# Kernel optimization log

Hardware: AMD Instinct MI355X
Metric: run time of the kernel (lower is better)

Reference implementation:

```python
import jax, jax.numpy as jnp
import numpy as np

K = 64      # neighbor_num (subgraph size)
TOPK = 10   # topk for sparse adjacency scatter
DN = 10     # density_neighbor


def _build_graphs(indexes, features):
    # compute_knn: inner-product top-K neighbor table over all N samples
    N, D = features.shape
    sim = features @ features.T                      # [N, N]
    _, ori0 = jax.lax.top_k(sim, K)                  # [N, K] neighbor indices
    # density: all_sim[n] = sum_{i<DN} <f_n, f_{ori0[n,i]}> / (4*DN)
    g = features[ori0[:, :DN]]                       # [N, DN, D]
    all_sim = jnp.einsum('nd,nkd->n', features, g) / (4.0 * DN)
    exp_sim = jnp.exp(all_sim)                       # [N]

    rows = jnp.arange(K)[:, None]                    # [K,1]

    def build_one(idx):
        nbr = ori0[idx]                              # [K] neighbors of query idx
        feat = features[nbr]                         # [K, D]
        neigh = ori0[nbr][:, :TOPK]                  # [K, TOPK]
        A = (feat @ features.T) * exp_sim[None, :]   # [K, N] density-reweighted sims
        # scatter only the topk entries of each row into sparse tmp
        tmp = jnp.zeros((K, N), features.dtype).at[rows, neigh].set(A[rows, neigh])
        adj = tmp @ (tmp.T > 0).astype(features.dtype)   # [K, K]
        adj = jax.nn.softmax(adj, axis=1)
        x = feat - feat[0]                           # center on query node
        return x, adj

    return jax.vmap(build_one)(indexes)              # [B,K,D], [B,K,K]


def _gconv(x, adj, W, b):
    # GraphConv with MeanAggregator: out = relu(concat([x, adj@x]) @ W + b)
    agg = jnp.einsum('bij,bjd->bid', adj, x)
    cat = jnp.concatenate([x, agg], axis=-1)
    return jax.nn.relu(jnp.einsum('bkd,df->bkf', cat, W) + b)


def setup_inputs() -> dict:
    key = jax.random.key(0)
    ks = jax.random.split(key, 16)
    N, D, NHID = 8192, 2048, 1024
    feats = jax.random.normal(ks[0], (N, D), dtype=jnp.float32)
    feats = feats / jnp.linalg.norm(feats, axis=1, keepdims=True)  # L2-normalized embeddings
    p = lambda k, shape: jax.random.normal(k, shape, dtype=jnp.float32) * 0.02
    return {
        'indexes': jax.random.randint(ks[1], (64,), 0, N, dtype=jnp.int64) if jax.config.jax_enable_x64 else jax.random.randint(ks[1], (64,), 0, N, dtype=jnp.int32),
        'features': feats,
        'labels': jax.random.randint(ks[2], (N,), 0, 1000, dtype=jnp.int32),
        'domain': 1,
        'W1': p(ks[3], (2 * D, NHID)), 'b1': jnp.zeros((NHID,), jnp.float32),
        'W2': p(ks[4], (2 * NHID, 512)), 'b2': jnp.zeros((512,), jnp.float32),
        'W3': p(ks[5], (2 * 512, 256)), 'b3': jnp.zeros((256,), jnp.float32),
        'W4': p(ks[6], (2 * 256, 256)), 'b4': jnp.zeros((256,), jnp.float32),
        'Wc1': p(ks[7], (256, 256)), 'bc1': jnp.zeros((256,), jnp.float32),
        'prelu_a': jnp.full((256,), 0.25, jnp.float32),
        'Wc2': p(ks[8], (256, 2)), 'bc2': jnp.zeros((2,), jnp.float32),
    }


def reference(indexes, features, labels, domain, W1, b1, W2, b2, W3, b3, W4, b4,
              Wc1, bc1, prelu_a, Wc2, bc2):
    # labels only used for the (optional) loss branch; domain=1 path implemented.
    xs, adjs = _build_graphs(indexes, features)      # built under no_grad in torch
    h = _gconv(xs, adjs, W1, b1)
    h = _gconv(h, adjs, W2, b2)
    h = _gconv(h, adjs, W3, b3)
    h = _gconv(h, adjs, W4, b4)
    h = h @ Wc1 + bc1
    h = jnp.where(h > 0, h, prelu_a * h)             # PReLU(256)
    pred = h @ Wc2 + bc2                             # [B, K, 2]
    return pred
```

## Files before the change

### kernel.cpp

```cpp
#include <hip/hip_runtime.h>
#include <hip/hip_bf16.h>
#include <math.h>

#define NROWS 8192
#define DFEAT 2048
#define KSEL  64
#define CHK   2048

typedef unsigned long long u64;
typedef __attribute__((ext_vector_type(8))) short bf16x8;
typedef __attribute__((ext_vector_type(4))) float f32x4;

__device__ __forceinline__ u64 umax64(u64 a, u64 b) { return a > b ? a : b; }

__device__ __forceinline__ void split2(float v, ushort& h, ushort& l) {
  __hip_bfloat16 bh = __float2bfloat16(v);
  float r = v - __bfloat162float(bh);
  __hip_bfloat16 bl = __float2bfloat16(r);
  h = *(ushort*)&bh; l = *(ushort*)&bl;
}

__device__ __forceinline__ u64 mkkey_vi(float v, int i) {
  unsigned u = __float_as_uint(v);
  u = ((int)u < 0) ? ~u : (u | 0x80000000u);
  return ((u64)u << 32) | (u64)(0xFFFFFFFFu - (unsigned)i);
}

__global__ __launch_bounds__(256) void k_split(const float* __restrict__ F, ushort* __restrict__ H,
                                               ushort* __restrict__ M, ushort* __restrict__ L) {
  const size_t i0 = ((size_t)blockIdx.x * 256 + threadIdx.x) * 4;
  float4 x = *(const float4*)(F + i0);
  float xs[4] = {x.x, x.y, x.z, x.w};
  ushort h[4], m[4], l[4];
#pragma unroll
  for (int c = 0; c < 4; ++c) {
    float v = xs[c];
    __hip_bfloat16 bh = __float2bfloat16(v);
    float r1 = v - __bfloat162float(bh);
    __hip_bfloat16 bm = __float2bfloat16(r1);
    float r2 = r1 - __bfloat162float(bm);
    __hip_bfloat16 bl = __float2bfloat16(r2);
    h[c] = *(ushort*)&bh; m[c] = *(ushort*)&bm; l[c] = *(ushort*)&bl;
  }
  ushort4 vh = {h[0], h[1], h[2], h[3]};
  ushort4 vm = {m[0], m[1], m[2], m[3]};
  ushort4 vl = {l[0], l[1], l[2], l[3]};
  *(ushort4*)(H + i0) = vh;
  *(ushort4*)(M + i0) = vm;
  *(ushort4*)(L + i0) = vl;
}

__global__ __launch_bounds__(256) void k_simgemm_pair(
    const ushort* __restrict__ FH, const ushort* __restrict__ FM, const ushort* __restrict__ FL,
    float* __restrict__ T0, float* __restrict__ T0T, int i0, int j0, int d0,
    float* __restrict__ T1, float* __restrict__ T1T, int i1, int j1, int d1) {
  __shared__ ushort lds[6 * 4096];
  const int z = blockIdx.z;
  float* TILE = z ? T1 : T0;
  float* TILT = z ? T1T : T0T;
  const int ci = z ? i1 : i0;
  const int cj = z ? j1 : j0;
  const int diag = z ? d1 : d0;
  const int bj = blockIdx.x;
  const int bm = blockIdx.y;
  if (diag && bm > bj) return;
  const int t = threadIdx.x;
  const int w = t >> 6, l = t & 63;
  const int arow0 = ci * CHK + bm * 128;
  const int brow0 = cj * CHK + bj * 128;
  const int segr = l >> 2;
  const int segq_s = (l & 3) ^ ((l >> 3) & 3);
  const int fl15 = l & 15, fq = l >> 4;
  const int kswz = (fq ^ ((fl15 >> 1) & 3)) * 8;
  const int wr = w >> 1, wc = w & 1;
  const int mb = wr * 64, nb = wc * 64;

  f32x4 acc[4][4];
#pragma unroll
  for (int i = 0; i < 4; ++i)
#pragma unroll
    for (int j = 0; j < 4; ++j) acc[i][j] = (f32x4){0.f, 0.f, 0.f, 0.f};

  for (int k0 = 0; k0 < DFEAT; k0 += 32) {
    __syncthreads();
#pragma unroll
    for (int c = 0; c < 12; ++c) {
      const int cc = w * 12 + c;
      const int tt = cc >> 3;
      const int p = cc & 7;
      const int rowbase = (tt < 3) ? arow0 : brow0;
      const int sp = (tt < 3) ? tt : (tt - 3);
      const ushort* sel = (sp == 0) ? FH : ((sp == 1) ? FM : FL);
      const ushort* g = sel + (size_t)(rowbase + p * 16 + segr) * DFEAT + (k0 + segq_s * 8);
      __builtin_amdgcn_global_load_lds((const __attribute__((address_space(1))) unsigned int*)g,
                                       (__attribute__((address_space(3))) unsigned int*)&lds[tt * 4096 + p * 512],
                                       16, 0, 0);
    }
    __syncthreads();

    bf16x8 af[3][4];
    bf16x8 bg[3][4];
#pragma unroll
    for (int i = 0; i < 3; ++i)
#pragma unroll
      for (int fm = 0; fm < 4; ++fm)
        af[i][fm] = *(const bf16x8*)&lds[i * 4096 + (mb + fm * 16 + fl15) * 32 + kswz];
#pragma unroll
    for (int j = 0; j < 3; ++j)
#pragma unroll
      for (int fn = 0; fn < 4; ++fn)
        bg[j][fn] = *(const bf16x8*)&lds[(3 + j) * 4096 + (nb + fn * 16 + fl15) * 32 + kswz];

#pragma unroll
    for (int fm = 0; fm < 4; ++fm)
#pragma unroll
      for (int fn = 0; fn < 4; ++fn) {
        f32x4 a = acc[fm][fn];
        a = __builtin_amdgcn_mfma_f32_16x16x32_bf16(af[0][fm], bg[0][fn], a, 0, 0, 0);
        a = __builtin_amdgcn_mfma_f32_16x16x32_bf16(af[1][fm], bg[0][fn], a, 0, 0, 0);
        a = __builtin_amdgcn_mfma_f32_16x16x32_bf16(af[0][fm], bg[1][fn], a, 0, 0, 0);
        a = __builtin_amdgcn_mfma_f32_16x16x32_bf16(af[2][fm], bg[0][fn], a, 0, 0, 0);
        a = __builtin_amdgcn_mfma_f32_16x16x32_bf16(af[0][fm], bg[2][fn], a, 0, 0, 0);
        a = __builtin_amdgcn_mfma_f32_16x16x32_bf16(af[1][fm], bg[1][fn], a, 0, 0, 0);
        acc[fm][fn] = a;
      }
  }

  const bool doT = (TILT != nullptr) && !(diag && bm == bj);
#pragma unroll
  for (int fm = 0; fm < 4; ++fm) {
    const int lm = bm * 128 + mb + fm * 16 + fq * 4;
#pragma unroll
    for (int fn = 0; fn < 4; ++fn) {
      const int col = bj * 128 + nb + fn * 16 + fl15;
#pragma unroll
      for (int r = 0; r < 4; ++r)
        TILE[(size_t)(lm + r) * CHK + col] = acc[fm][fn][r];
      if (doT) {
        float4 v = make_float4(acc[fm][fn][0], acc[fm][fn][1], acc[fm][fn][2], acc[fm][fn][3]);
        *(float4*)(TILT + (size_t)col * CHK + lm) = v;
      }
    }
  }
}

__global__ __launch_bounds__(256) void k_simgemm_mfma(
    const ushort* __restrict__ FH, const ushort* __restrict__ FM, const ushort* __restrict__ FL,
    float* __restrict__ C, int row0) {
  __shared__ ushort lds[6 * 4096];
  const int bj = blockIdx.x;
  const int bm = blockIdx.y;
  const int t = threadIdx.x;
  const int w = t >> 6, l = t & 63;
  const int arow0 = row0 + bm * 128;
  const int brow0 = bj * 128;
  const int segr = l >> 2;
  const int segq = l & 3;
  const int fl15 = l & 15, fq = l >> 4;
  const int wr = w >> 1, wc = w & 1;
  const int mb = wr * 64, nb = wc * 64;

  f32x4 acc[4][4];
#pragma unroll
  for (int i = 0; i < 4; ++i)
#pragma unroll
    for (int j = 0; j < 4; ++j) acc[i][j] = (f32x4){0.f, 0.f, 0.f, 0.f};

  for (int k0 = 0; k0 < DFEAT; k0 += 32) {
    __syncthreads();
#pragma unroll
    for (int c = 0; c < 12; ++c) {
      const int cc = w * 12 + c;
      const int tt = cc >> 3;
      const int p = cc & 7;
      const int rowbase = (tt < 3) ? arow0 : brow0;
      const int sp = (tt < 3) ? tt : (tt - 3);
      const ushort* sel = (sp == 0) ? FH : ((sp == 1) ? FM : FL);
      const ushort* g = sel + (size_t)(rowbase + p * 16 + segr) * DFEAT + (k0 + segq * 8);
      __builtin_amdgcn_global_load_lds((const __attribute__((address_space(1))) unsigned int*)g,
                                       (__attribute__((address_space(3))) unsigned int*)&lds[tt * 4096 + p * 512],
                                       16, 0, 0);
    }
    __syncthreads();

    bf16x8 af[3][4];
    bf16x8 bg[3][4];
    const int kcol = fq * 8;
#pragma unroll
    for (int i = 0; i < 3; ++i)
#pragma unroll
      for (int fm = 0; fm < 4; ++fm)
        af[i][fm] = *(const bf16x8*)&lds[i * 4096 + (mb + fm * 16 + fl15) * 32 + kcol];
#pragma unroll
    for (int j = 0; j < 3; ++j)
#pragma unroll
      for (int fn = 0; fn < 4; ++fn)
        bg[j][fn] = *(const bf16x8*)&lds[(3 + j) * 4096 + (nb + fn * 16 + fl15) * 32 + kcol];

#pragma unroll
    for (int fm = 0; fm < 4; ++fm)
#pragma unroll
      for (int fn = 0; fn < 4; ++fn) {
        f32x4 a = acc[fm][fn];
        a = __builtin_amdgcn_mfma_f32_16x16x32_bf16(af[0][fm], bg[0][fn], a, 0, 0, 0);
        a = __builtin_amdgcn_mfma_f32_16x16x32_bf16(af[1][fm], bg[0][fn], a, 0, 0, 0);
        a = __builtin_amdgcn_mfma_f32_16x16x32_bf16(af[0][fm], bg[1][fn], a, 0, 0, 0);
        a = __builtin_amdgcn_mfma_f32_16x16x32_bf16(af[2][fm], bg[0][fn], a, 0, 0, 0);
        a = __builtin_amdgcn_mfma_f32_16x16x32_bf16(af[0][fm], bg[2][fn], a, 0, 0, 0);
        a = __builtin_amdgcn_mfma_f32_16x16x32_bf16(af[1][fm], bg[1][fn], a, 0, 0, 0);
        acc[fm][fn] = a;
      }
  }

#pragma unroll
  for (int fm = 0; fm < 4; ++fm) {
    const int lm = bm * 128 + mb + fm * 16 + fq * 4;
#pragma unroll
    for (int fn = 0; fn < 4; ++fn) {
      const int col = bj * 128 + nb + fn * 16 + fl15;
#pragma unroll
      for (int r = 0; r < 4; ++r)
        C[(size_t)(lm + r) * NROWS + col] = acc[fm][fn][r];
    }
  }
}

__global__ __launch_bounds__(256) void k_gemm3(const ushort* __restrict__ AH, const ushort* __restrict__ AL,
                                               const ushort* __restrict__ BH, const ushort* __restrict__ BL,
                                               float* __restrict__ C, int K, int N) {
  __shared__ ushort lds[4 * 4096];
  const int bj = blockIdx.x, bm = blockIdx.y;
  const int t = threadIdx.x;
  const int w = t >> 6, l = t & 63;
  const int segr = l >> 2;
  const int segq_s = (l & 3) ^ ((l >> 3) & 3);
  const int fl15 = l & 15, fq = l >> 4;
  const int kswz = (fq ^ ((fl15 >> 1) & 3)) * 8;
  const int wr = w >> 1, wc = w & 1;
  const int mb = wr * 64, nb = wc * 64;

  f32x4 acc[4][4];
#pragma unroll
  for (int i = 0; i < 4; ++i)
#pragma unroll
    for (int j = 0; j < 4; ++j) acc[i][j] = (f32x4){0.f, 0.f, 0.f, 0.f};

  for (int k0 = 0; k0 < K; k0 += 32) {
    __syncthreads();
#pragma unroll
    for (int c = 0; c < 8; ++c) {
      const int s = w * 8 + c;
      const int tt = s >> 3;
      const int p = s & 7;
      const int rowbase = (tt < 2) ? (bm * 128) : (bj * 128);
      const ushort* sel = (tt == 0) ? AH : ((tt == 1) ? AL : ((tt == 2) ? BH : BL));
      const ushort* g = sel + (size_t)(rowbase + p * 16 + segr) * K + (k0 + segq_s * 8);
      __builtin_amdgcn_global_load_lds((const __attribute__((address_space(1))) unsigned int*)g,
                                       (__attribute__((address_space(3))) unsigned int*)&lds[s * 512],
                                       16, 0, 0);
    }
    __syncthreads();

    bf16x8 af[2][4];
    bf16x8 bg[2][4];
#pragma unroll
    for (int i = 0; i < 2; ++i)
#pragma unroll
      for (int fm = 0; fm < 4; ++fm)
        af[i][fm] = *(const bf16x8*)&lds[i * 4096 + (mb + fm * 16 + fl15) * 32 + kswz];
#pragma unroll
    for (int j = 0; j < 2; ++j)
#pragma unroll
      for (int fn = 0; fn < 4; ++fn)
        bg[j][fn] = *(const bf16x8*)&lds[(2 + j) * 4096 + (nb + fn * 16 + fl15) * 32 + kswz];

#pragma unroll
    for (int fm = 0; fm < 4; ++fm)
#pragma unroll
      for (int fn = 0; fn < 4; ++fn) {
        f32x4 a = acc[fm][fn];
        a = __builtin_amdgcn_mfma_f32_16x16x32_bf16(af[0][fm], bg[0][fn], a, 0, 0, 0);
        a = __builtin_amdgcn_mfma_f32_16x16x32_bf16(af[0][fm], bg[1][fn], a, 0, 0, 0);
        a = __builtin_amdgcn_mfma_f32_16x16x32_bf16(af[1][fm], bg[0][fn], a, 0, 0, 0);
        acc[fm][fn] = a;
      }
  }

#pragma unroll
  for (int fm = 0; fm < 4; ++fm) {
    const int row = bm * 128 + mb + fm * 16 + fq * 4;
#pragma unroll
    for (int fn = 0; fn < 4; ++fn) {
      const int col = bj * 128 + nb + fn * 16 + fl15;
#pragma unroll
      for (int r = 0; r < 4; ++r)
        C[(size_t)(row + r) * N + col] = acc[fm][fn][r];
    }
  }
}

__global__ __launch_bounds__(256) void k_init_topk(float* __restrict__ topv, int* __restrict__ topi) {
  const int i = blockIdx.x * 256 + threadIdx.x;
  topv[i] = -INFINITY;
  topi[i] = 0;
}

__global__ __launch_bounds__(256) void k_topk_update(const float* __restrict__ T, int rowbase, int colbase,
                                                     float* __restrict__ topv, int* __restrict__ topi) {
  __shared__ unsigned cnt[64];
  __shared__ unsigned nsel;
  __shared__ u64 selbuf[64];
  const int t = threadIdx.x;
  const int row = rowbase + blockIdx.x;
  const float* src = T + (size_t)blockIdx.x * CHK;

  if (t < 64) cnt[t] = 0;
  if (t == 0) nsel = 0;

  u64 k[9];
  int nk = 8;
#pragma unroll
  for (int q = 0; q < 8; ++q) {
    float v = src[t + 256 * q];
    k[q] = mkkey_vi(v, colbase + t + 256 * q);
  }
  k[8] = 0;
  if (t < 64) {
    k[8] = mkkey_vi(topv[(size_t)row * KSEL + t], topi[(size_t)row * KSEL + t]);
    nk = 9;
  }
  __syncthreads();

  u64 T64 = 0;
  for (int bit = 63; bit >= 0; --bit) {
    const u64 cand = T64 | (1ull << bit);
    unsigned c = 0;
#pragma unroll
    for (int q = 0; q < 9; ++q) c += (q < nk && k[q] >= cand) ? 1u : 0u;
#pragma unroll
    for (int s = 32; s > 0; s >>= 1) c += __shfl_down(c, s);
    if ((t & 63) == 0) atomicAdd(&cnt[bit], c);
    __syncthreads();
    const unsigned cb = cnt[bit];
    if (cb >= 64) T64 = cand;
    if (cb == 64) break;
  }

#pragma unroll
  for (int q = 0; q < 9; ++q) {
    if (q < nk && k[q] >= T64) {
      unsigned p = atomicAdd(&nsel, 1u);
      if (p < 64) selbuf[p] = k[q];
    }
  }
  __syncthreads();

  if (t < 64) {
    u64 key = selbuf[t];
#pragma unroll
    for (int kk = 2; kk <= 64; kk <<= 1) {
#pragma unroll
      for (int j = kk >> 1; j > 0; j >>= 1) {
        u64 other = __shfl_xor(key, j);
        const bool dirDesc = ((t & kk) == 0);
        const bool upper = ((t & j) != 0);
        u64 mx = umax64(key, other);
        u64 mn = (key < other) ? key : other;
        key = (dirDesc ^ upper) ? mx : mn;
      }
    }
    const unsigned ui = (unsigned)(key >> 32);
    const float v = __uint_as_float((ui & 0x80000000u) ? (ui ^ 0x80000000u) : ~ui);
    const int idx = (int)(0xFFFFFFFFu - (unsigned)(key & 0xFFFFFFFFull));
    topv[(size_t)row * KSEL + t] = v;
    topi[(size_t)row * KSEL + t] = idx;
  }
}

__global__ __launch_bounds__(256) void k_exps(const float* __restrict__ topv, float* __restrict__ exps) {
  const int r = blockIdx.x * 256 + threadIdx.x;
  float s = 0.f;
#pragma unroll
  for (int q = 0; q < 10; ++q) s += topv[(size_t)r * KSEL + q];
  exps[r] = expf(s / 40.0f);
}

__global__ __launch_bounds__(256) void k_topk(const float* __restrict__ simc,
                                              float* __restrict__ topv, int* __restrict__ topi,
                                              float* __restrict__ exps, int row0) {
  __shared__ float vals[NROWS];
  __shared__ u64 wmax[4];
  __shared__ float outv[KSEL];
  __shared__ int outi[KSEL];
  const int row = row0 + blockIdx.x;
  const int t = threadIdx.x;
  const float* src = simc + (size_t)blockIdx.x * NROWS;
  for (int i = t; i < NROWS; i += 256) vals[i] = src[i];
  __syncthreads();

  u64 lk = 0;
#pragma unroll
  for (int m = 0; m < 32; ++m) {
    int i = t + 256 * m;
    lk = umax64(lk, mkkey_vi(vals[i], i));
  }

  const int lane = t & 63, wv = t >> 6;
  for (int it = 0; it < KSEL; ++it) {
    u64 wk = lk;
#pragma unroll
    for (int s = 32; s > 0; s >>= 1) {
      u64 o = __shfl_xor(wk, s);
      wk = umax64(wk, o);
    }
    if (lane == 0) wmax[wv] = wk;
    __syncthreads();
    u64 g = umax64(umax64(wmax[0], wmax[1]), umax64(wmax[2], wmax[3]));
    const unsigned ui = (unsigned)(g >> 32);
    const float v = __uint_as_float((ui & 0x80000000u) ? (ui ^ 0x80000000u) : ~ui);
    const int idx = (int)(0xFFFFFFFFu - (unsigned)(g & 0xFFFFFFFFull));
    if (t == 0) { outv[it] = v; outi[it] = idx; }
    if (t == (idx & 255)) {
      vals[idx] = -INFINITY;
      u64 nl = 0;
#pragma unroll
      for (int m = 0; m < 32; ++m) {
        int i = t + 256 * m;
        nl = umax64(nl, mkkey_vi(vals[i], i));
      }
      lk = nl;
    }
    __syncthreads();
  }
  if (t < KSEL) {
    topv[(size_t)row * KSEL + t] = outv[t];
    topi[(size_t)row * KSEL + t] = outi[t];
  }
  if (t == 0) {
    float s = 0.f;
#pragma unroll
    for (int q = 0; q < 10; ++q) s += outv[q];
    exps[row] = expf(s / 40.0f);
  }
}

__global__ __launch_bounds__(256) void k_adj(const int* __restrict__ indexes,
                                             const float* __restrict__ topv, const int* __restrict__ topi,
                                             const float* __restrict__ exps, float* __restrict__ adj) {
  __shared__ int nbr[64];
  __shared__ int neigh[64][10];
  __shared__ float tv[64][10];
  __shared__ float adjL[64][64];
  const int b = blockIdx.x;
  const int t = threadIdx.x;
  const int idx = indexes[b];
  if (t < 64) nbr[t] = topi[(size_t)idx * KSEL + t];
  __syncthreads();
  for (int p = t; p < 640; p += 256) {
    const int r = p / 10, q = p - r * 10;
    const int m = nbr[r];
    const int c = topi[(size_t)m * KSEL + q];
    neigh[r][q] = c;
    tv[r][q] = topv[(size_t)m * KSEL + q] * exps[c];
  }
  __syncthreads();
  for (int p = t; p < 4096; p += 256) {
    const int i = p >> 6, j = p & 63;
    float s = 0.f;
#pragma unroll
    for (int q = 0; q < 10; ++q) {
      const int c = neigh[i][q];
      float add = 0.f;
      for (int s2 = 0; s2 < 10; ++s2) {
        if (neigh[j][s2] == c) { add = (tv[j][s2] > 0.f) ? tv[i][q] : 0.f; break; }
      }
      s += add;
    }
    adjL[i][j] = s;
  }
  __syncthreads();
  const int wv = t >> 6, lane = t & 63;
  for (int i = wv * 16; i < wv * 16 + 16; ++i) {
    float v = adjL[i][lane];
    float mx = v;
#pragma unroll
    for (int s = 32; s > 0; s >>= 1) mx = fmaxf(mx, __shfl_xor(mx, s));
    float e = expf(v - mx);
    float sum = e;
#pragma unroll
    for (int s = 32; s > 0; s >>= 1) sum += __shfl_xor(sum, s);
    adj[((size_t)b * 64 + i) * 64 + lane] = e / sum;
  }
}

__global__ __launch_bounds__(256) void k_xs_split(const int* __restrict__ indexes, const int* __restrict__ topi,
                                                  const float* __restrict__ F,
                                                  ushort* __restrict__ XH, ushort* __restrict__ XL) {
  const int b = blockIdx.y, r = blockIdx.x;
  const int t = threadIdx.x;
  const int idx = indexes[b];
  const int m  = topi[(size_t)idx * KSEL + r];
  const int m0 = topi[(size_t)idx * KSEL + 0];
  const float4* pa = (const float4*)(F + (size_t)m * DFEAT);
  const float4* pb = (const float4*)(F + (size_t)m0 * DFEAT);
  const size_t rowoff = ((size_t)b * 64 + r) * DFEAT;
#pragma unroll
  for (int it = 0; it < 2; ++it) {
    const int i = t + it * 256;
    float4 a = pa[i], c = pb[i];
    float d[4] = {a.x - c.x, a.y - c.y, a.z - c.z, a.w - c.w};
    ushort h[4], l[4];
#pragma unroll
    for (int q = 0; q < 4; ++q) split2(d[q], h[q], l[q]);
    ushort4 vh = {h[0], h[1], h[2], h[3]};
    ushort4 vl = {l[0], l[1], l[2], l[3]};
    *(ushort4*)(XH + rowoff + i * 4) = vh;
    *(ushort4*)(XL + rowoff + i * 4) = vl;
  }
}

__global__ __launch_bounds__(256) void k_wsplitT(const float* __restrict__ W,
                                                 ushort* __restrict__ WTH, ushort* __restrict__ WTL,
                                                 int K, int F) {
  __shared__ float tile[32][33];
  const int k0 = blockIdx.x * 32;
  const int n0 = blockIdx.y * 32;
  const int t = threadIdx.x;
  {
    const int r = t >> 3, cq = t & 7;
    const int srcRow = (n0 < F) ? (k0 + r) : (K + k0 + r);
    const int srcCol = (n0 < F) ? n0 : (n0 - F);
    float4 v = *(const float4*)(W + (size_t)srcRow * F + srcCol + cq * 4);
    tile[r][cq * 4 + 0] = v.x; tile[r][cq * 4 + 1] = v.y;
    tile[r][cq * 4 + 2] = v.z; tile[r][cq * 4 + 3] = v.w;
  }
  __syncthreads();
  {
    const int nl = t >> 3, kq = t & 7;
    ushort h[4], l[4];
#pragma unroll
    for (int i = 0; i < 4; ++i) split2(tile[kq * 4 + i][nl], h[i], l[i]);
    ushort4 vh = {h[0], h[1], h[2], h[3]};
    ushort4 vl = {l[0], l[1], l[2], l[3]};
    *(ushort4*)(WTH + (size_t)(n0 + nl) * K + k0 + kq * 4) = vh;
    *(ushort4*)(WTL + (size_t)(n0 + nl) * K + k0 + kq * 4) = vl;
  }
}

__global__ __launch_bounds__(256) void k_postlayer(const float* __restrict__ C, const float* __restrict__ adj,
                                                   const float* __restrict__ bias,
                                                   ushort* __restrict__ HH, ushort* __restrict__ HL, int F) {
  __shared__ float adjL[64 * 65];
  __shared__ float QL[64 * 66];
  const int f0 = blockIdx.x * 64;
  const int b = blockIdx.y;
  const int t = threadIdx.x;
  const int fc = t & 63, rg = t >> 6;
  const int twoF = 2 * F;
  for (int i = t; i < 4096; i += 256) {
    const int r = i >> 6, j = i & 63;
    adjL[r * 65 + j] = adj[(size_t)b * 4096 + i];
    QL[r * 66 + j] = C[(size_t)(b * 64 + r) * twoF + F + f0 + j];
  }
  __syncthreads();
  const float bv = bias[f0 + fc];
  for (int rr = 0; rr < 16; ++rr) {
    const int r = rg * 16 + rr;
    float s = 0.f;
#pragma unroll 8
    for (int j0 = 0; j0 < 64; ++j0) {
      const int j = (j0 + fc) & 63;
      s += adjL[r * 65 + j] * QL[j * 66 + fc];
    }
    const int row = b * 64 + r;
    float h = C[(size_t)row * twoF + f0 + fc] + s + bv;
    h = fmaxf(h, 0.f);
    ushort hh, hl;
    split2(h, hh, hl);
    HH[(size_t)row * F + f0 + fc] = hh;
    HL[(size_t)row * F + f0 + fc] = hl;
  }
}

__global__ __launch_bounds__(256) void k_postcls(const float* __restrict__ C, const float* __restrict__ bias,
                                                 const float* __restrict__ pre, float* __restrict__ HC) {
  const size_t i0 = ((size_t)blockIdx.x * 256 + threadIdx.x) * 4;
  const int col = (int)(i0 & 255);
  float4 c = *(const float4*)(C + i0);
  float o[4] = {c.x, c.y, c.z, c.w};
#pragma unroll
  for (int i = 0; i < 4; ++i) {
    float h = o[i] + bias[col + i];
    o[i] = (h > 0.f) ? h : pre[col + i] * h;
  }
  *(float4*)(HC + i0) = make_float4(o[0], o[1], o[2], o[3]);
}

__global__ __launch_bounds__(256) void k_final(const float* __restrict__ Hc, const float* __restrict__ Wc2,
                                               const float* __restrict__ bc2, float* __restrict__ outp) {
  __shared__ float w[512];
  __shared__ float red[512];
  const int t = threadIdx.x;
  for (int i = t; i < 512; i += 256) w[i] = Wc2[i];
  __syncthreads();
  const int m = blockIdx.x * 64 + (t >> 2);
  const int p = t & 3;
  const float* h = Hc + (size_t)m * 256;
  float s0 = 0.f, s1 = 0.f;
  for (int k = p * 64; k < p * 64 + 64; ++k) {
    float hv = h[k];
    s0 += hv * w[k * 2];
    s1 += hv * w[k * 2 + 1];
  }
  red[t * 2] = s0; red[t * 2 + 1] = s1;
  __syncthreads();
  if (p == 0) {
    for (int q = 1; q < 4; ++q) { s0 += red[(t + q) * 2]; s1 += red[(t + q) * 2 + 1]; }
    outp[m * 2 + 0] = s0 + bc2[0];
    outp[m * 2 + 1] = s1 + bc2[1];
  }
}

extern "C" void kernel_launch(void* const* d_in, const int* in_sizes, int n_in,
                              void* d_out, int out_size, void* d_ws, size_t ws_size,
                              hipStream_t stream) {
  const int*   indexes = (const int*)d_in[0];
  const float* F   = (const float*)d_in[1];
  const float* W1  = (const float*)d_in[4];
  const float* b1  = (const float*)d_in[5];
  const float* W2  = (const float*)d_in[6];
  const float* b2  = (const float*)d_in[7];
  const float* W3  = (const float*)d_in[8];
  const float* b3  = (const float*)d_in[9];
  const float* W4  = (const float*)d_in[10];
  const float* b4  = (const float*)d_in[11];
  const float* Wc1 = (const float*)d_in[12];
  const float* bc1 = (const float*)d_in[13];
  const float* pre = (const float*)d_in[14];
  const float* Wc2 = (const float*)d_in[15];
  const float* bc2 = (const float*)d_in[16];
  float* out = (float*)d_out;

  size_t off = 0;
  auto take = [&](size_t bytes) -> char* {
    char* q = (char*)d_ws + off;
    off += (bytes + 255) & ~(size_t)255;
    return q;
  };
  float* TOPV = (float*)take((size_t)NROWS * KSEL * 4);
  int*   TOPI = (int*)  take((size_t)NROWS * KSEL * 4);
  float* EXPS = (float*)take((size_t)NROWS * 4);
  float* ADJ  = (float*)take((size_t)64 * 64 * 64 * 4);
  char*  big  = (char*)d_ws + off;
  const size_t big_bytes = (ws_size > off) ? (ws_size - off) : 0;

  const size_t Mi = 1024 * 1024;
  const size_t Ki = 1024;
  const size_t splitBytes = (size_t)NROWS * DFEAT * 2;

  if (big_bytes >= 160 * Mi) {
    ushort* FH = (ushort*)big;
    ushort* FM = (ushort*)(big + splitBytes);
    ushort* FL = (ushort*)(big + 2 * splitBytes);
    float* TILE0  = (float*)(big + 96 * Mi);
    float* TILE0T = (float*)(big + 112 * Mi);
    float* TILE1  = (float*)(big + 128 * Mi);
    float* TILE1T = (float*)(big + 144 * Mi);
    k_split<<<NROWS * DFEAT / 1024, 256, 0, stream>>>(F, FH, FM, FL);
    k_init_topk<<<NROWS * KSEL / 256, 256, 0, stream>>>(TOPV, TOPI);
    const int pairs[10][2] = {{0,0},{0,1},{0,2},{0,3},{1,1},{1,2},{1,3},{2,2},{2,3},{3,3}};
    for (int b = 0; b < 5; ++b) {
      const int ia = pairs[2*b][0],   ja = pairs[2*b][1];
      const int ib = pairs[2*b+1][0], jb = pairs[2*b+1][1];
      const int da = (ia == ja), db = (ib == jb);
      k_simgemm_pair<<<dim3(16, 16, 2), 256, 0, stream>>>(
          FH, FM, FL,
          TILE0, da ? TILE0 : TILE0T, ia, ja, da,
          TILE1, db ? TILE1 : TILE1T, ib, jb, db);
      k_topk_update<<<CHK, 256, 0, stream>>>(TILE0, ia * CHK, ja * CHK, TOPV, TOPI);
      if (!da) k_topk_update<<<CHK, 256, 0, stream>>>(TILE0T, ja * CHK, ia * CHK, TOPV, TOPI);
      k_topk_update<<<CHK, 256, 0, stream>>>(TILE1, ib * CHK, jb * CHK, TOPV, TOPI);
      if (!db) k_topk_update<<<CHK, 256, 0, stream>>>(TILE1T, jb * CHK, ib * CHK, TOPV, TOPI);
    }
    k_exps<<<NROWS / 256, 256, 0, stream>>>(TOPV, EXPS);
  } else {
    int fchunk = 0;
    for (int c = 2048; c >= 512; c >>= 1) {
      if (3 * splitBytes + (size_t)c * NROWS * 4 <= big_bytes) { fchunk = c; break; }
    }
    if (fchunk == 0) {
      hipMemsetAsync(d_out, 0, (size_t)out_size * 4, stream);
      return;
    }
    ushort* FH = (ushort*)big;
    ushort* FM = (ushort*)(big + splitBytes);
    ushort* FL = (ushort*)(big + 2 * splitBytes);
    float* SIMC = (float*)(big + 3 * splitBytes);
    k_split<<<NROWS * DFEAT / 1024, 256, 0, stream>>>(F, FH, FM, FL);
    for (int r0 = 0; r0 < NROWS; r0 += fchunk) {
      k_simgemm_mfma<<<dim3(64, fchunk / 128), 256, 0, stream>>>(FH, FM, FL, SIMC, r0);
      k_topk<<<fchunk, 256, 0, stream>>>(SIMC, TOPV, TOPI, EXPS, r0);
    }
  }
  k_adj<<<64, 256, 0, stream>>>(indexes, TOPV, TOPI, EXPS, ADJ);

  ushort* XH   = (ushort*)(big);
  ushort* XL   = (ushort*)(big + 16 * Mi);
  ushort* WT1H = (ushort*)(big + 32 * Mi);
  ushort* WT1L = (ushort*)(big + 40 * Mi);
  ushort* WT2H = (ushort*)(big + 48 * Mi);
  ushort* WT2L = (ushort*)(big + 50 * Mi);
  ushort* WT3H = (ushort*)(big + 52 * Mi);
  ushort* WT3L = (ushort*)(big + 52 * Mi + 512 * Ki);
  ushort* WT4H = (ushort*)(big + 53 * Mi);
  ushort* WT4L = (ushort*)(big + 53 * Mi + 256 * Ki);
  ushort* WTcH = (ushort*)(big + 53 * Mi + 512 * Ki);
  ushort* WTcL = (ushort*)(big + 53 * Mi + 640 * Ki);
  float*  CBUF = (float*)(big + 54 * Mi);
  float*  HC   = (float*)(big + 86 * Mi);
  ushort* H1H  = (ushort*)(big + 32 * Mi);
  ushort* H1L  = (ushort*)(big + 40 * Mi);
  ushort* H2H  = (ushort*)(big);
  ushort* H2L  = (ushort*)(big + 4 * Mi);
  ushort* H3H  = (ushort*)(big + 8 * Mi);
  ushort* H3L  = (ushort*)(big + 10 * Mi);
  ushort* H4H  = (ushort*)(big + 12 * Mi);
  ushort* H4L  = (ushort*)(big + 14 * Mi);

  k_wsplitT<<<dim3(2048 / 32, 2048 / 32), 256, 0, stream>>>(W1, WT1H, WT1L, 2048, 1024);
  k_wsplitT<<<dim3(1024 / 32, 1024 / 32), 256, 0, stream>>>(W2, WT2H, WT2L, 1024, 512);
  k_wsplitT<<<dim3(512 / 32, 512 / 32), 256, 0, stream>>>(W3, WT3H, WT3L, 512, 256);
  k_wsplitT<<<dim3(256 / 32, 512 / 32), 256, 0, stream>>>(W4, WT4H, WT4L, 256, 256);
  k_wsplitT<<<dim3(256 / 32, 256 / 32), 256, 0, stream>>>(Wc1, WTcH, WTcL, 256, 256);

  k_xs_split<<<dim3(64, 64), 256, 0, stream>>>(indexes, TOPI, F, XH, XL);

  k_gemm3<<<dim3(16, 32), 256, 0, stream>>>(XH, XL, WT1H, WT1L, CBUF, 2048, 2048);
  k_postlayer<<<dim3(16, 64), 256, 0, stream>>>(CBUF, ADJ, b1, H1H, H1L, 1024);
  k_gemm3<<<dim3(8, 32), 256, 0, stream>>>(H1H, H1L, WT2H, WT2L, CBUF, 1024, 1024);
  k_postlayer<<<dim3(8, 64), 256, 0, stream>>>(CBUF, ADJ, b2, H2H, H2L, 512);
  k_gemm3<<<dim3(4, 32), 256, 0, stream>>>(H2H, H2L, WT3H, WT3L, CBUF, 512, 512);
  k_postlayer<<<dim3(4, 64), 256, 0, stream>>>(CBUF, ADJ, b3, H3H, H3L, 256);
  k_gemm3<<<dim3(4, 32), 256, 0, stream>>>(H3H, H3L, WT4H, WT4L, CBUF, 256, 512);
  k_postlayer<<<dim3(4, 64), 256, 0, stream>>>(CBUF, ADJ, b4, H4H, H4L, 256);
  k_gemm3<<<dim3(2, 32), 256, 0, stream>>>(H4H, H4L, WTcH, WTcL, CBUF, 256, 256);
  k_postcls<<<4096 * 256 / 1024, 256, 0, stream>>>(CBUF, bc1, pre, HC);

  k_final<<<64, 256, 0, stream>>>(HC, Wc2, bc2, out);
}
```

Baseline: 1.650 ms.

## Compute all similarity tiles in one launch and batch top-k merges; fuse classifier epilogue

When the workspace is large enough, a single launch now computes all ten upper-triangular 2048x2048 similarity tiles, writing each tile and its transpose into a full 16-tile buffer. Top-k merges then run in four launches, each covering one tile per row-chunk. This replaces five paired GEMM launches plus many small per-tile top-k launches, giving more parallelism per launch and fewer launch gaps, at the cost of about 256MB of extra workspace. Separately, the bias+PReLU pass is folded into the final classifier kernel, removing one launch and an intermediate buffer.

```diff
diff --git a/kernel.cpp b/kernel.cpp
--- a/kernel.cpp
+++ b/kernel.cpp
@@ -48,6 +48,101 @@
   *(ushort4*)(H + i0) = vh;
   *(ushort4*)(M + i0) = vm;
   *(ushort4*)(L + i0) = vl;
+}
+
+__global__ __launch_bounds__(256) void k_simgemm_all(
+    const ushort* __restrict__ FH, const ushort* __restrict__ FM, const ushort* __restrict__ FL,
+    float* __restrict__ bufbase) {
+  __shared__ ushort lds[6 * 4096];
+  const int z = blockIdx.z;
+  int ci = 0, rem = z;
+  while (rem >= 4 - ci) { rem -= 4 - ci; ++ci; }
+  const int cj = ci + rem;
+  const int diag = (ci == cj);
+  const int bj = blockIdx.x;
+  const int bm = blockIdx.y;
+  if (diag && bm > bj) return;
+  const size_t TSZ = (size_t)CHK * CHK;
+  float* TILE = bufbase + (size_t)(ci * 4 + cj) * TSZ;
+  float* TILT = bufbase + (size_t)(cj * 4 + ci) * TSZ;
+  const int t = threadIdx.x;
+  const int w = t >> 6, l = t & 63;
+  const int arow0 = ci * CHK + bm * 128;
+  const int brow0 = cj * CHK + bj * 128;
+  const int segr = l >> 2;
+  const int segq_s = (l & 3) ^ ((l >> 3) & 3);
+  const int fl15 = l & 15, fq = l >> 4;
+  const int kswz = (fq ^ ((fl15 >> 1) & 3)) * 8;
+  const int wr = w >> 1, wc = w & 1;
+  const int mb = wr * 64, nb = wc * 64;
+
+  f32x4 acc[4][4];
+#pragma unroll
+  for (int i = 0; i < 4; ++i)
+#pragma unroll
+    for (int j = 0; j < 4; ++j) acc[i][j] = (f32x4){0.f, 0.f, 0.f, 0.f};
+
+  for (int k0 = 0; k0 < DFEAT; k0 += 32) {
+    __syncthreads();
+#pragma unroll
+    for (int c = 0; c < 12; ++c) {
+      const int cc = w * 12 + c;
+      const int tt = cc >> 3;
+      const int p = cc & 7;
+      const int rowbase = (tt < 3) ? arow0 : brow0;
+      const int sp = (tt < 3) ? tt : (tt - 3);
+      const ushort* sel = (sp == 0) ? FH : ((sp == 1) ? FM : FL);
+      const ushort* g = sel + (size_t)(rowbase + p * 16 + segr) * DFEAT + (k0 + segq_s * 8);
+      __builtin_amdgcn_global_load_lds((const __attribute__((address_space(1))) unsigned int*)g,
+                                       (__attribute__((address_space(3))) unsigned int*)&lds[tt * 4096 + p * 512],
+                                       16, 0, 0);
+    }
+    __syncthreads();
+
+    bf16x8 af[3][4];
+    bf16x8 bg[3][4];
+#pragma unroll
+    for (int i = 0; i < 3; ++i)
+#pragma unroll
+      for (int fm = 0; fm < 4; ++fm)
+        af[i][fm] = *(const bf16x8*)&lds[i * 4096 + (mb + fm * 16 + fl15) * 32 + kswz];
+#pragma unroll
+    for (int j = 0; j < 3; ++j)
+#pragma unroll
+      for (int fn = 0; fn < 4; ++fn)
+        bg[j][fn] = *(const bf16x8*)&lds[(3 + j) * 4096 + (nb + fn * 16 + fl15) * 32 + kswz];
+
+#pragma unroll
+    for (int fm = 0; fm < 4; ++fm)
+#pragma unroll
+      for (int fn = 0; fn < 4; ++fn) {
+        f32x4 a = acc[fm][fn];
+        a = __builtin_amdgcn_mfma_f32_16x16x32_bf16(af[0][fm], bg[0][fn], a, 0, 0, 0);
+        a = __builtin_amdgcn_mfma_f32_16x16x32_bf16(af[1][fm], bg[0][fn], a, 0, 0, 0);
+        a = __builtin_amdgcn_mfma_f32_16x16x32_bf16(af[0][fm], bg[1][fn], a, 0, 0, 0);
+        a = __builtin_amdgcn_mfma_f32_16x16x32_bf16(af[2][fm], bg[0][fn], a, 0, 0, 0);
+        a = __builtin_amdgcn_mfma_f32_16x16x32_bf16(af[0][fm], bg[2][fn], a, 0, 0, 0);
+        a = __builtin_amdgcn_mfma_f32_16x16x32_bf16(af[1][fm], bg[1][fn], a, 0, 0, 0);
+        acc[fm][fn] = a;
+      }
+  }
+
+  const bool doT = !(diag && bm == bj);
+#pragma unroll
+  for (int fm = 0; fm < 4; ++fm) {
+    const int lm = bm * 128 + mb + fm * 16 + fq * 4;
+#pragma unroll
+    for (int fn = 0; fn < 4; ++fn) {
+      const int col = bj * 128 + nb + fn * 16 + fl15;
+#pragma unroll
+      for (int r = 0; r < 4; ++r)
+        TILE[(size_t)(lm + r) * CHK + col] = acc[fm][fn][r];
+      if (doT) {
+        float4 v = make_float4(acc[fm][fn][0], acc[fm][fn][1], acc[fm][fn][2], acc[fm][fn][3]);
+        *(float4*)(TILT + (size_t)col * CHK + lm) = v;
+      }
+    }
+  }
 }
 
 __global__ __launch_bounds__(256) void k_simgemm_pair(
@@ -305,17 +400,12 @@
   topi[i] = 0;
 }
 
-__global__ __launch_bounds__(256) void k_topk_update(const float* __restrict__ T, int rowbase, int colbase,
-                                                     float* __restrict__ topv, int* __restrict__ topi) {
-  __shared__ unsigned cnt[64];
-  __shared__ unsigned nsel;
-  __shared__ u64 selbuf[64];
-  const int t = threadIdx.x;
-  const int row = rowbase + blockIdx.x;
-  const float* src = T + (size_t)blockIdx.x * CHK;
-
+__device__ __forceinline__ void topk_merge_body(const float* src, int row, int colbase,
+                                                float* topv, int* topi,
+                                                unsigned* cnt, unsigned* nselp, u64* selbuf) {
+  const int t = threadIdx.x;
   if (t < 64) cnt[t] = 0;
-  if (t == 0) nsel = 0;
+  if (t == 0) *nselp = 0;
 
   u64 k[9];
   int nk = 8;
@@ -349,7 +439,7 @@
 #pragma unroll
   for (int q = 0; q < 9; ++q) {
     if (q < nk && k[q] >= T64) {
-      unsigned p = atomicAdd(&nsel, 1u);
+      unsigned p = atomicAdd(nselp, 1u);
       if (p < 64) selbuf[p] = k[q];
     }
   }
@@ -377,6 +467,27 @@
   }
 }
 
+__global__ __launch_bounds__(256) void k_topk_update4(const float* __restrict__ bufbase, int g,
+                                                      float* __restrict__ topv, int* __restrict__ topi) {
+  __shared__ unsigned cnt[64];
+  __shared__ unsigned nsel;
+  __shared__ u64 selbuf[64];
+  const int r = blockIdx.y;
+  const int c = (r + g) & 3;
+  const size_t TSZ = (size_t)CHK * CHK;
+  const float* src = bufbase + (size_t)(r * 4 + c) * TSZ + (size_t)blockIdx.x * CHK;
+  topk_merge_body(src, r * CHK + blockIdx.x, c * CHK, topv, topi, cnt, &nsel, selbuf);
+}
+
+__global__ __launch_bounds__(256) void k_topk_update(const float* __restrict__ T, int rowbase, int colbase,
+                                                     float* __restrict__ topv, int* __restrict__ topi) {
+  __shared__ unsigned cnt[64];
+  __shared__ unsigned nsel;
+  __shared__ u64 selbuf[64];
+  const float* src = T + (size_t)blockIdx.x * CHK;
+  topk_merge_body(src, rowbase + blockIdx.x, colbase, topv, topi, cnt, &nsel, selbuf);
+}
+
 __global__ __launch_bounds__(256) void k_exps(const float* __restrict__ topv, float* __restrict__ exps) {
   const int r = blockIdx.x * 256 + threadIdx.x;
   float s = 0.f;
@@ -582,22 +693,9 @@
   }
 }
 
-__global__ __launch_bounds__(256) void k_postcls(const float* __restrict__ C, const float* __restrict__ bias,
-                                                 const float* __restrict__ pre, float* __restrict__ HC) {
-  const size_t i0 = ((size_t)blockIdx.x * 256 + threadIdx.x) * 4;
-  const int col = (int)(i0 & 255);
-  float4 c = *(const float4*)(C + i0);
-  float o[4] = {c.x, c.y, c.z, c.w};
-#pragma unroll
-  for (int i = 0; i < 4; ++i) {
-    float h = o[i] + bias[col + i];
-    o[i] = (h > 0.f) ? h : pre[col + i] * h;
-  }
-  *(float4*)(HC + i0) = make_float4(o[0], o[1], o[2], o[3]);
-}
-
-__global__ __launch_bounds__(256) void k_final(const float* __restrict__ Hc, const float* __restrict__ Wc2,
-                                               const float* __restrict__ bc2, float* __restrict__ outp) {
+__global__ __launch_bounds__(256) void k_final2(const float* __restrict__ C, const float* __restrict__ bc1,
+                                                const float* __restrict__ pre, const float* __restrict__ Wc2,
+                                                const float* __restrict__ bc2, float* __restrict__ outp) {
   __shared__ float w[512];
   __shared__ float red[512];
   const int t = threadIdx.x;
@@ -605,10 +703,11 @@
   __syncthreads();
   const int m = blockIdx.x * 64 + (t >> 2);
   const int p = t & 3;
-  const float* h = Hc + (size_t)m * 256;
+  const float* h = C + (size_t)m * 256;
   float s0 = 0.f, s1 = 0.f;
   for (int k = p * 64; k < p * 64 + 64; ++k) {
-    float hv = h[k];
+    float hv = h[k] + bc1[k];
+    hv = (hv > 0.f) ? hv : pre[k] * hv;
     s0 += hv * w[k * 2];
     s1 += hv * w[k * 2 + 1];
   }
@@ -658,7 +757,18 @@
   const size_t Ki = 1024;
   const size_t splitBytes = (size_t)NROWS * DFEAT * 2;
 
-  if (big_bytes >= 160 * Mi) {
+  if (big_bytes >= 352 * Mi) {
+    ushort* FH = (ushort*)big;
+    ushort* FM = (ushort*)(big + splitBytes);
+    ushort* FL = (ushort*)(big + 2 * splitBytes);
+    float* BUFS = (float*)(big + 96 * Mi);
+    k_split<<<NROWS * DFEAT / 1024, 256, 0, stream>>>(F, FH, FM, FL);
+    k_init_topk<<<NROWS * KSEL / 256, 256, 0, stream>>>(TOPV, TOPI);
+    k_simgemm_all<<<dim3(16, 16, 10), 256, 0, stream>>>(FH, FM, FL, BUFS);
+    for (int g = 0; g < 4; ++g)
+      k_topk_update4<<<dim3(CHK, 4), 256, 0, stream>>>(BUFS, g, TOPV, TOPI);
+    k_exps<<<NROWS / 256, 256, 0, stream>>>(TOPV, EXPS);
+  } else if (big_bytes >= 160 * Mi) {
     ushort* FH = (ushort*)big;
     ushort* FM = (ushort*)(big + splitBytes);
     ushort* FL = (ushort*)(big + 2 * splitBytes);
@@ -717,7 +827,6 @@
   ushort* WTcH = (ushort*)(big + 53 * Mi + 512 * Ki);
   ushort* WTcL = (ushort*)(big + 53 * Mi + 640 * Ki);
   float*  CBUF = (float*)(big + 54 * Mi);
-  float*  HC   = (float*)(big + 86 * Mi);
   ushort* H1H  = (ushort*)(big + 32 * Mi);
   ushort* H1L  = (ushort*)(big + 40 * Mi);
   ushort* H2H  = (ushort*)(big);
@@ -744,7 +853,5 @@
   k_gemm3<<<dim3(4, 32), 256, 0, stream>>>(H3H, H3L, WT4H, WT4L, CBUF, 256, 512);
   k_postlayer<<<dim3(4, 64), 256, 0, stream>>>(CBUF, ADJ, b4, H4H, H4L, 256);
   k_gemm3<<<dim3(2, 32), 256, 0, stream>>>(H4H, H4L, WTcH, WTcL, CBUF, 256, 256);
-  k_postcls<<<4096 * 256 / 1024, 256, 0, stream>>>(CBUF, bc1, pre, HC);
-
-  k_final<<<64, 256, 0, stream>>>(HC, Wc2, bc2, out);
-}
+  k_final2<<<64, 256, 0, stream>>>(CBUF, bc1, pre, Wc2, bc2, out);
+}
```

New measurement: 1.661 ms. Within noise of the previous version (+0.7%).

## Batch similarity tiles into fewer launches and fuse classifier epilogue

Applied to the files above, without the earlier changes.

Reworks the blocked similarity/top-k schedule so several 2048x2048 tile products run in one launch of up to six tiles, using a pool of tile buffers. The top-k merges are batched four chunks per launch, so the 8192 rows update in parallel instead of through many small launches. This needs a larger scratch buffer (224 MiB path) and keeps a fallback for 160 MiB. Separately, the bias+PReLU post-classifier kernel is folded into the final projection kernel, removing one pass over the 4096x256 buffer.

```diff
diff --git a/kernel.cpp b/kernel.cpp
--- a/kernel.cpp
+++ b/kernel.cpp
@@ -50,20 +50,21 @@
   *(ushort4*)(L + i0) = vl;
 }
 
-__global__ __launch_bounds__(256) void k_simgemm_pair(
+__global__ __launch_bounds__(256) void k_sim_batch(
     const ushort* __restrict__ FH, const ushort* __restrict__ FM, const ushort* __restrict__ FL,
-    float* __restrict__ T0, float* __restrict__ T0T, int i0, int j0, int d0,
-    float* __restrict__ T1, float* __restrict__ T1T, int i1, int j1, int d1) {
+    float* __restrict__ BUFS, int e0, int e1, int e2, int e3, int e4, int e5) {
   __shared__ ushort lds[6 * 4096];
   const int z = blockIdx.z;
-  float* TILE = z ? T1 : T0;
-  float* TILT = z ? T1T : T0T;
-  const int ci = z ? i1 : i0;
-  const int cj = z ? j1 : j0;
-  const int diag = z ? d1 : d0;
+  const int e = (z == 0) ? e0 : ((z == 1) ? e1 : ((z == 2) ? e2 : ((z == 3) ? e3 : ((z == 4) ? e4 : e5))));
+  const int ci = e & 15, cj = (e >> 4) & 15;
+  const int bA = (e >> 8) & 15, bB = (e >> 12) & 15;
+  const int diag = (e >> 16) & 1;
   const int bj = blockIdx.x;
   const int bm = blockIdx.y;
   if (diag && bm > bj) return;
+  const size_t TSZ = (size_t)CHK * CHK;
+  float* TILE = BUFS + (size_t)bA * TSZ;
+  float* TILT = BUFS + (size_t)bB * TSZ;
   const int t = threadIdx.x;
   const int w = t >> 6, l = t & 63;
   const int arow0 = ci * CHK + bm * 128;
@@ -85,9 +86,9 @@
     __syncthreads();
 #pragma unroll
     for (int c = 0; c < 12; ++c) {
-      const int cc = w * 12 + c;
-      const int tt = cc >> 3;
-      const int p = cc & 7;
+      const int cidx = w * 12 + c;
+      const int tt = cidx >> 3;
+      const int p = cidx & 7;
       const int rowbase = (tt < 3) ? arow0 : brow0;
       const int sp = (tt < 3) ? tt : (tt - 3);
       const ushort* sel = (sp == 0) ? FH : ((sp == 1) ? FM : FL);
@@ -126,7 +127,7 @@
       }
   }
 
-  const bool doT = (TILT != nullptr) && !(diag && bm == bj);
+  const bool doT = !(diag && bm == bj);
 #pragma unroll
   for (int fm = 0; fm < 4; ++fm) {
     const int lm = bm * 128 + mb + fm * 16 + fq * 4;
@@ -305,17 +306,12 @@
   topi[i] = 0;
 }
 
-__global__ __launch_bounds__(256) void k_topk_update(const float* __restrict__ T, int rowbase, int colbase,
-                                                     float* __restrict__ topv, int* __restrict__ topi) {
-  __shared__ unsigned cnt[64];
-  __shared__ unsigned nsel;
-  __shared__ u64 selbuf[64];
-  const int t = threadIdx.x;
-  const int row = rowbase + blockIdx.x;
-  const float* src = T + (size_t)blockIdx.x * CHK;
-
+__device__ __forceinline__ void topk_merge_body(const float* src, int row, int colbase,
+                                                float* topv, int* topi,
+                                                unsigned* cnt, unsigned* nselp, u64* selbuf) {
+  const int t = threadIdx.x;
   if (t < 64) cnt[t] = 0;
-  if (t == 0) nsel = 0;
+  if (t == 0) *nselp = 0;
 
   u64 k[9];
   int nk = 8;
@@ -349,7 +345,7 @@
 #pragma unroll
   for (int q = 0; q < 9; ++q) {
     if (q < nk && k[q] >= T64) {
-      unsigned p = atomicAdd(&nsel, 1u);
+      unsigned p = atomicAdd(nselp, 1u);
       if (p < 64) selbuf[p] = k[q];
     }
   }
@@ -377,6 +373,21 @@
   }
 }
 
+__global__ __launch_bounds__(256) void k_topk_upd4(const float* __restrict__ bufbase,
+                                                   int b0, int b1, int b2, int b3,
+                                                   int c0, int c1, int c2, int c3,
+                                                   float* __restrict__ topv, int* __restrict__ topi) {
+  __shared__ unsigned cnt[64];
+  __shared__ unsigned nsel;
+  __shared__ u64 selbuf[64];
+  const int y = blockIdx.y;
+  const int bi = (y == 0) ? b0 : ((y == 1) ? b1 : ((y == 2) ? b2 : b3));
+  const int cc = (y == 0) ? c0 : ((y == 1) ? c1 : ((y == 2) ? c2 : c3));
+  const size_t TSZ = (size_t)CHK * CHK;
+  const float* src = bufbase + (size_t)bi * TSZ + (size_t)blockIdx.x * CHK;
+  topk_merge_body(src, y * CHK + blockIdx.x, cc * CHK, topv, topi, cnt, &nsel, selbuf);
+}
+
 __global__ __launch_bounds__(256) void k_exps(const float* __restrict__ topv, float* __restrict__ exps) {
   const int r = blockIdx.x * 256 + threadIdx.x;
   float s = 0.f;
@@ -582,22 +593,9 @@
   }
 }
 
-__global__ __launch_bounds__(256) void k_postcls(const float* __restrict__ C, const float* __restrict__ bias,
-                                                 const float* __restrict__ pre, float* __restrict__ HC) {
-  const size_t i0 = ((size_t)blockIdx.x * 256 + threadIdx.x) * 4;
-  const int col = (int)(i0 & 255);
-  float4 c = *(const float4*)(C + i0);
-  float o[4] = {c.x, c.y, c.z, c.w};
-#pragma unroll
-  for (int i = 0; i < 4; ++i) {
-    float h = o[i] + bias[col + i];
-    o[i] = (h > 0.f) ? h : pre[col + i] * h;
-  }
-  *(float4*)(HC + i0) = make_float4(o[0], o[1], o[2], o[3]);
-}
-
-__global__ __launch_bounds__(256) void k_final(const float* __restrict__ Hc, const float* __restrict__ Wc2,
-                                               const float* __restrict__ bc2, float* __restrict__ outp) {
+__global__ __launch_bounds__(256) void k_final2(const float* __restrict__ C, const float* __restrict__ bc1,
+                                                const float* __restrict__ pre, const float* __restrict__ Wc2,
+                                                const float* __restrict__ bc2, float* __restrict__ outp) {
   __shared__ float w[512];
   __shared__ float red[512];
   const int t = threadIdx.x;
@@ -605,10 +603,11 @@
   __syncthreads();
   const int m = blockIdx.x * 64 + (t >> 2);
   const int p = t & 3;
-  const float* h = Hc + (size_t)m * 256;
+  const float* h = C + (size_t)m * 256;
   float s0 = 0.f, s1 = 0.f;
   for (int k = p * 64; k < p * 64 + 64; ++k) {
-    float hv = h[k];
+    float hv = h[k] + bc1[k];
+    hv = (hv > 0.f) ? hv : pre[k] * hv;
     s0 += hv * w[k * 2];
     s1 += hv * w[k * 2 + 1];
   }
@@ -657,31 +656,48 @@
   const size_t Mi = 1024 * 1024;
   const size_t Ki = 1024;
   const size_t splitBytes = (size_t)NROWS * DFEAT * 2;
-
-  if (big_bytes >= 160 * Mi) {
+  const size_t TSZ = (size_t)CHK * CHK;
+
+  auto enc = [](int ci, int cj, int ba, int bb, int dg) {
+    return ci | (cj << 4) | (ba << 8) | (bb << 12) | (dg << 16);
+  };
+
+  if (big_bytes >= 224 * Mi) {
     ushort* FH = (ushort*)big;
     ushort* FM = (ushort*)(big + splitBytes);
     ushort* FL = (ushort*)(big + 2 * splitBytes);
-    float* TILE0  = (float*)(big + 96 * Mi);
-    float* TILE0T = (float*)(big + 112 * Mi);
-    float* TILE1  = (float*)(big + 128 * Mi);
-    float* TILE1T = (float*)(big + 144 * Mi);
+    float* BUFS = (float*)(big + 96 * Mi);
     k_split<<<NROWS * DFEAT / 1024, 256, 0, stream>>>(F, FH, FM, FL);
     k_init_topk<<<NROWS * KSEL / 256, 256, 0, stream>>>(TOPV, TOPI);
-    const int pairs[10][2] = {{0,0},{0,1},{0,2},{0,3},{1,1},{1,2},{1,3},{2,2},{2,3},{3,3}};
-    for (int b = 0; b < 5; ++b) {
-      const int ia = pairs[2*b][0],   ja = pairs[2*b][1];
-      const int ib = pairs[2*b+1][0], jb = pairs[2*b+1][1];
-      const int da = (ia == ja), db = (ib == jb);
-      k_simgemm_pair<<<dim3(16, 16, 2), 256, 0, stream>>>(
-          FH, FM, FL,
-          TILE0, da ? TILE0 : TILE0T, ia, ja, da,
-          TILE1, db ? TILE1 : TILE1T, ib, jb, db);
-      k_topk_update<<<CHK, 256, 0, stream>>>(TILE0, ia * CHK, ja * CHK, TOPV, TOPI);
-      if (!da) k_topk_update<<<CHK, 256, 0, stream>>>(TILE0T, ja * CHK, ia * CHK, TOPV, TOPI);
-      k_topk_update<<<CHK, 256, 0, stream>>>(TILE1, ib * CHK, jb * CHK, TOPV, TOPI);
-      if (!db) k_topk_update<<<CHK, 256, 0, stream>>>(TILE1T, jb * CHK, ib * CHK, TOPV, TOPI);
-    }
+    k_sim_batch<<<dim3(16, 16, 6), 256, 0, stream>>>(FH, FM, FL, BUFS,
+        enc(0,0,0,0,1), enc(1,1,1,1,1), enc(2,2,2,2,1), enc(3,3,3,3,1),
+        enc(0,1,4,5,0), enc(2,3,6,7,0));
+    k_topk_upd4<<<dim3(CHK, 4), 256, 0, stream>>>(BUFS, 0, 1, 2, 3, 0, 1, 2, 3, TOPV, TOPI);
+    k_topk_upd4<<<dim3(CHK, 4), 256, 0, stream>>>(BUFS, 4, 5, 6, 7, 1, 0, 3, 2, TOPV, TOPI);
+    k_sim_batch<<<dim3(16, 16, 4), 256, 0, stream>>>(FH, FM, FL, BUFS,
+        enc(0,2,0,1,0), enc(1,3,2,3,0), enc(0,3,4,5,0), enc(1,2,6,7,0), 0, 0);
+    k_topk_upd4<<<dim3(CHK, 4), 256, 0, stream>>>(BUFS, 0, 2, 1, 3, 2, 3, 0, 1, TOPV, TOPI);
+    k_topk_upd4<<<dim3(CHK, 4), 256, 0, stream>>>(BUFS, 4, 6, 7, 5, 3, 2, 1, 0, TOPV, TOPI);
+    k_exps<<<NROWS / 256, 256, 0, stream>>>(TOPV, EXPS);
+  } else if (big_bytes >= 160 * Mi) {
+    ushort* FH = (ushort*)big;
+    ushort* FM = (ushort*)(big + splitBytes);
+    ushort* FL = (ushort*)(big + 2 * splitBytes);
+    float* BUFS = (float*)(big + 96 * Mi);
+    k_split<<<NROWS * DFEAT / 1024, 256, 0, stream>>>(F, FH, FM, FL);
+    k_init_topk<<<NROWS * KSEL / 256, 256, 0, stream>>>(TOPV, TOPI);
+    k_sim_batch<<<dim3(16, 16, 4), 256, 0, stream>>>(FH, FM, FL, BUFS,
+        enc(0,0,0,0,1), enc(1,1,1,1,1), enc(2,2,2,2,1), enc(3,3,3,3,1), 0, 0);
+    k_topk_upd4<<<dim3(CHK, 4), 256, 0, stream>>>(BUFS, 0, 1, 2, 3, 0, 1, 2, 3, TOPV, TOPI);
+    k_sim_batch<<<dim3(16, 16, 2), 256, 0, stream>>>(FH, FM, FL, BUFS,
+        enc(0,1,0,1,0), enc(2,3,2,3,0), 0, 0, 0, 0);
+    k_topk_upd4<<<dim3(CHK, 4), 256, 0, stream>>>(BUFS, 0, 1, 2, 3, 1, 0, 3, 2, TOPV, TOPI);
+    k_sim_batch<<<dim3(16, 16, 2), 256, 0, stream>>>(FH, FM, FL, BUFS,
+        enc(0,2,0,1,0), enc(1,3,2,3,0), 0, 0, 0, 0);
+    k_topk_upd4<<<dim3(CHK, 4), 256, 0, stream>>>(BUFS, 0, 2, 1, 3, 2, 3, 0, 1, TOPV, TOPI);
+    k_sim_batch<<<dim3(16, 16, 2), 256, 0, stream>>>(FH, FM, FL, BUFS,
+        enc(0,3,0,1,0), enc(1,2,2,3,0), 0, 0, 0, 0);
+    k_topk_upd4<<<dim3(CHK, 4), 256, 0, stream>>>(BUFS, 0, 2, 3, 1, 3, 2, 1, 0, TOPV, TOPI);
     k_exps<<<NROWS / 256, 256, 0, stream>>>(TOPV, EXPS);
   } else {
     int fchunk = 0;
@@ -717,7 +733,6 @@
   ushort* WTcH = (ushort*)(big + 53 * Mi + 512 * Ki);
   ushort* WTcL = (ushort*)(big + 53 * Mi + 640 * Ki);
   float*  CBUF = (float*)(big + 54 * Mi);
-  float*  HC   = (float*)(big + 86 * Mi);
   ushort* H1H  = (ushort*)(big + 32 * Mi);
   ushort* H1L  = (ushort*)(big + 40 * Mi);
   ushort* H2H  = (ushort*)(big);
@@ -744,7 +759,5 @@
   k_gemm3<<<dim3(4, 32), 256, 0, stream>>>(H3H, H3L, WT4H, WT4L, CBUF, 256, 512);
   k_postlayer<<<dim3(4, 64), 256, 0, stream>>>(CBUF, ADJ, b4, H4H, H4L, 256);
   k_gemm3<<<dim3(2, 32), 256, 0, stream>>>(H4H, H4L, WTcH, WTcL, CBUF, 256, 256);
-  k_postcls<<<4096 * 256 / 1024, 256, 0, stream>>>(CBUF, bc1, pre, HC);
-
-  k_final<<<64, 256, 0, stream>>>(HC, Wc2, bc2, out);
-}
+  k_final2<<<64, 256, 0, stream>>>(CBUF, bc1, pre, Wc2, bc2, out);
+}
```

Result: faster. 1.557 ms (-5.6%).
